# Performance work log

Measured on AMD Instinct MI355X. Metric: run time of the kernel, lower is better.

The kernel has to match this reference:

```python
import jax, jax.numpy as jnp
import numpy as np

B, C, N, OUT, K = 8, 64, 4096, 64, 16


def setup_inputs() -> dict:
    key = jax.random.key(0)
    k0, k1, k2, k3, k4 = jax.random.split(key, 5)
    x = jax.random.normal(k0, (B, C, N, 1), jnp.float32)
    s1 = 1.0 / np.sqrt(2 * C)
    s2 = 1.0 / np.sqrt(OUT)
    W1 = jax.random.uniform(k1, (2 * C, OUT), jnp.float32, -s1, s1)
    b1 = jax.random.uniform(k2, (OUT,), jnp.float32, -s1, s1)
    W2 = jax.random.uniform(k3, (OUT, OUT), jnp.float32, -s2, s2)
    b2 = jax.random.uniform(k4, (OUT,), jnp.float32, -s2, s2)
    return {"x": x, "W1": W1, "b1": b1, "W2": W2, "b2": b2}


def reference(x, W1, b1, W2, b2):
    # x: [B, C, N, 1] -> node features [B, N, C]
    xb = x[..., 0].transpose(0, 2, 1)  # [B, N, C]
    # kNN per batch element (PyG knn includes the point itself)
    sq = jnp.sum(xb * xb, axis=-1)  # [B, N]
    d2 = sq[:, :, None] + sq[:, None, :] - 2.0 * jnp.einsum('bnc,bmc->bnm', xb, xb)
    _, idx = jax.lax.top_k(-d2, K)  # [B, N, K] neighbor indices
    # gather neighbor features: [B, N, K, C]
    xj = jax.vmap(lambda f, i: jnp.take(f, i, axis=0))(xb, idx)
    xi = xb[:, :, None, :]  # [B, N, 1, C]
    # EdgeConv edge features: [x_i, x_j - x_i]
    e = jnp.concatenate([jnp.broadcast_to(xi, xj.shape), xj - xi], axis=-1)  # [B,N,K,2C]
    h = jax.nn.relu(e @ W1 + b1)
    h = jax.nn.relu(h @ W2 + b2)
    out = jnp.max(h, axis=2)  # max aggregation over neighbors -> [B, N, OUT]
    return out.transpose(0, 2, 1)[..., None]  # [B, OUT, N, 1]
```

## Files before the change

kernel.cpp:

```cpp
#include <hip/hip_runtime.h>
#include <stdint.h>

#define BB 8
#define CCH 64
#define NPB 4096
#define NPTS (BB*NPB)
#define PPW 8

typedef float  f32x2  __attribute__((ext_vector_type(2)));
typedef float  f32x4v __attribute__((ext_vector_type(4)));
typedef short  bf16x8 __attribute__((ext_vector_type(8)));
typedef unsigned short u16x8 __attribute__((ext_vector_type(8)));
typedef unsigned long long u64;
typedef unsigned int u32;

__device__ __forceinline__ unsigned short f2bf(float x) {
    u32 u = __float_as_uint(x);
    u += 0x7FFFu + ((u >> 16) & 1u);
    return (unsigned short)(u >> 16);
}

template<typename T>
__device__ __forceinline__ void sort16(T* key) {
#pragma unroll
    for (int kk = 2; kk <= 16; kk <<= 1) {
#pragma unroll
        for (int j = kk >> 1; j > 0; j >>= 1) {
#pragma unroll
            for (int i = 0; i < 16; ++i) {
                int l = i ^ j;
                if (l > i) {
                    bool up = ((i & kk) == 0);
                    T a = key[i], c = key[l];
                    bool cond = up ? (c < a) : (a < c);
                    key[i] = cond ? c : a;
                    key[l] = cond ? a : c;
                }
            }
        }
    }
}

template<typename T>
__device__ __forceinline__ void merge16(T* list, const T* key) {
    T m[16];
#pragma unroll
    for (int i = 0; i < 16; ++i) {
        T a = list[i], c = key[15 - i];
        m[i] = (c < a) ? c : a;
    }
#pragma unroll
    for (int j = 8; j > 0; j >>= 1) {
#pragma unroll
        for (int i = 0; i < 16; ++i) {
            if ((i & j) == 0) {
                T a = m[i], c = m[i + j];
                bool cond = c < a;
                m[i]     = cond ? c : a;
                m[i + j] = cond ? a : c;
            }
        }
    }
#pragma unroll
    for (int i = 0; i < 16; ++i) list[i] = m[i];
}

__global__ void k_transpose(const float* __restrict__ x, float* __restrict__ xb,
                            unsigned short* __restrict__ xh, float* __restrict__ sq) {
    __shared__ float tile[64][65];
    int b  = blockIdx.y;
    int n0 = blockIdx.x * 64;
    int tx = threadIdx.x, ty = threadIdx.y;
    const float* xp = x + (size_t)b * CCH * NPB;
#pragma unroll
    for (int r = 0; r < 8; ++r) {
        int c = ty + r * 8;
        tile[c][tx] = xp[(size_t)c * NPB + n0 + tx];
    }
    __syncthreads();
    float* xbp = xb + ((size_t)b * NPB + n0) * CCH;
    unsigned short* xhp = xh + ((size_t)b * NPB + n0) * CCH;
    float* sqp = sq + (size_t)b * NPB + n0;
#pragma unroll
    for (int r = 0; r < 8; ++r) {
        int nn = ty + r * 8;
        float v = tile[tx][nn];
        xbp[(size_t)nn * CCH + tx] = v;
        xhp[(size_t)nn * CCH + tx] = f2bf(v);
        float s = v * v;
#pragma unroll
        for (int o = 32; o > 0; o >>= 1) s += __shfl_xor(s, o);
        if (tx == 0) sqp[nn] = s;
    }
}

__global__ void k_prepw(const float* __restrict__ W1, const float* __restrict__ W2,
                        unsigned short* __restrict__ W1t, unsigned short* __restrict__ W2t) {
    int t = blockIdx.x * 256 + threadIdx.x;
    if (t < 8192) {
        int o = t >> 7, k = t & 127;
        float v = (k < 64) ? (W1[k * 64 + o] - W1[(64 + k) * 64 + o]) : W1[k * 64 + o];
        W1t[o * 128 + k] = f2bf(v);
    } else if (t < 12288) {
        int u = t - 8192;
        int o = u >> 6, j = u & 63;
        W2t[o * 64 + j] = f2bf(W2[j * 64 + o]);
    }
}

__global__ __launch_bounds__(256) void k_gemm(const unsigned short* __restrict__ xh,
                                              const float* __restrict__ sq,
                                              u32* __restrict__ cand) {
    __shared__ float dtile[64][65];
    __shared__ u32 llist[64][65];
    int b = blockIdx.y >> 6;
    const unsigned short* xhB = xh + (size_t)b * NPB * CCH;
    const float* sqB = sq + (size_t)b * NPB;
    u32* candB = cand + (size_t)b * 64 * NPB * 16;
    int l = threadIdx.x & 63;
    int w = threadIdx.x >> 6;
    int m0 = (blockIdx.y & 63) * 64;
    int n0 = blockIdx.x * 64;
    const unsigned short* ap = xhB + (size_t)(m0 + w * 16 + (l & 15)) * CCH + ((l >> 4) * 8);
    bf16x8 a0 = *(const bf16x8*)ap;
    bf16x8 a1 = *(const bf16x8*)(ap + 32);
    f32x4v z = {0.f, 0.f, 0.f, 0.f};
    f32x4v acc[4];
#pragma unroll
    for (int cg = 0; cg < 4; ++cg) {
        const unsigned short* bp = xhB + (size_t)(n0 + cg * 16 + (l & 15)) * CCH + ((l >> 4) * 8);
        bf16x8 b0 = *(const bf16x8*)bp;
        bf16x8 b1 = *(const bf16x8*)(bp + 32);
        acc[cg] = __builtin_amdgcn_mfma_f32_16x16x32_bf16(a0, b0, z, 0, 0, 0);
        acc[cg] = __builtin_amdgcn_mfma_f32_16x16x32_bf16(a1, b1, acc[cg], 0, 0, 0);
    }
    int rb = m0 + w * 16 + (l >> 4) * 4;
    float4 sr = *(const float4*)(sqB + rb);
    float sqr[4] = {sr.x, sr.y, sr.z, sr.w};
#pragma unroll
    for (int cg = 0; cg < 4; ++cg) {
        int cit = cg * 16 + (l & 15);
        float sc = sqB[n0 + cit];
#pragma unroll
        for (int j = 0; j < 4; ++j) {
            float v = fmaxf(fmaf(-2.f, acc[cg][j], sqr[j] + sc), 0.f);
            dtile[w * 16 + (l >> 4) * 4 + j][cit] = v;
        }
    }
    __syncthreads();
    {
        int row = l, ch = w;
        u32 key[16];
#pragma unroll
        for (int e = 0; e < 16; ++e) {
            float v = dtile[row][ch * 16 + e];
            key[e] = ((u32)f2bf(v) << 16) | (u32)(n0 + ch * 16 + e);
        }
        sort16(key);
#pragma unroll
        for (int i = 0; i < 16; ++i) llist[row][ch * 16 + i] = key[i];
    }
    __syncthreads();
    if (threadIdx.x < 64) {
        int r2 = threadIdx.x;
        u32 list[16], tmp[16];
#pragma unroll
        for (int i = 0; i < 16; ++i) list[i] = llist[r2][i];
#pragma unroll
        for (int ch2 = 1; ch2 < 4; ++ch2) {
#pragma unroll
            for (int i = 0; i < 16; ++i) tmp[i] = llist[r2][ch2 * 16 + i];
            merge16(list, tmp);
        }
        u32* cp = candB + ((size_t)blockIdx.x * NPB + (m0 + r2)) * 16;
#pragma unroll
        for (int i = 0; i < 16; ++i) cp[i] = list[i];
    }
}

__global__ __launch_bounds__(256, 1) void k_post(const u32* __restrict__ cand,
                                                 const float* __restrict__ xb,
                                                 const float* __restrict__ sq,
                                                 int* __restrict__ idxo) {
    __shared__ u32 slots[4][64];
    int l  = threadIdx.x & 63;
    int rl = __builtin_amdgcn_readfirstlane(threadIdx.x >> 6);
    int rowg = blockIdx.x * 4 + rl;
    int b    = rowg >> 12;
    int row  = rowg & 4095;
    const float* xbB = xb + ((size_t)b << 12) * CCH;
    const float* sqB = sq + ((size_t)b << 12);
    const u32* candB = cand + (size_t)b * 64 * NPB * 16;
    const float* xr = xbB + (size_t)row * CCH;
    float rr[64];
#pragma unroll
    for (int i = 0; i < 16; ++i) {
        float4 v = *(const float4*)(xr + i * 4);
        rr[4*i] = v.x; rr[4*i+1] = v.y; rr[4*i+2] = v.z; rr[4*i+3] = v.w;
    }
    u32 karr[16];
    {
        const uint4* cp = (const uint4*)(candB + ((size_t)l * NPB + row) * 16);
#pragma unroll
        for (int i = 0; i < 4; ++i) {
            uint4 v = cp[i];
            karr[4*i] = v.x; karr[4*i+1] = v.y; karr[4*i+2] = v.z; karr[4*i+3] = v.w;
        }
    }
    u32 lo = 0, hi = 0xFFFFu;
#pragma unroll
    for (int it = 0; it < 16; ++it) {
        u32 mid = (lo + hi) >> 1;
        int c = 0;
#pragma unroll
        for (int i = 0; i < 16; ++i) c += ((karr[i] >> 16) <= mid) ? 1 : 0;
#pragma unroll
        for (int o = 32; o > 0; o >>= 1) c += __shfl_xor(c, o);
        bool ge = (c >= 48);
        lo = ge ? lo : (mid + 1);
        hi = ge ? mid : hi;
    }
    u32 vstar = hi;
    int cnt = 0;
#pragma unroll
    for (int i = 0; i < 16; ++i) cnt += ((karr[i] >> 16) <= vstar) ? 1 : 0;
    int pre = cnt;
#pragma unroll
    for (int d = 1; d < 64; d <<= 1) {
        int t = __shfl_up(pre, d);
        if (l >= d) pre += t;
    }
    int base = pre - cnt;
    u32* sl = slots[rl];
    sl[l] = 0xFFFFFFFFu;
#pragma unroll
    for (int i = 0; i < 16; ++i) {
        if (i < cnt) {
            int s = base + i;
            if (s < 64) sl[s] = karr[i];
        }
    }
    u32 mk = sl[l];
    u64 key = ~0ULL;
    if (mk != 0xFFFFFFFFu) {
        int col = (int)(mk & 0xFFFFu);
        const float* xj = xbB + (size_t)col * CCH;
        float lod = 0.f, hid = 0.f;
#pragma unroll
        for (int q = 0; q < 8; ++q) {
            float4 v  = *(const float4*)(xj + q * 4);
            float4 wv = *(const float4*)(xj + 32 + q * 4);
            lod = fmaf(v.x,  rr[4*q+0], lod);
            lod = fmaf(v.y,  rr[4*q+1], lod);
            lod = fmaf(v.z,  rr[4*q+2], lod);
            lod = fmaf(v.w,  rr[4*q+3], lod);
            hid = fmaf(wv.x, rr[32+4*q+0], hid);
            hid = fmaf(wv.y, rr[32+4*q+1], hid);
            hid = fmaf(wv.z, rr[32+4*q+2], hid);
            hid = fmaf(wv.w, rr[32+4*q+3], hid);
        }
        float d = fmaf(-2.f, lod + hid, sqB[col]);
        u32 fb = __float_as_uint(d);
        fb ^= (fb >> 31) ? 0xFFFFFFFFu : 0x80000000u;
        key = ((u64)fb << 32) | (u32)col;
    }
#pragma unroll
    for (int kk = 2; kk <= 64; kk <<= 1) {
#pragma unroll
        for (int j = kk >> 1; j > 0; j >>= 1) {
            u64 p = (u64)__shfl_xor((long long)key, j);
            bool keep_min = (((l & kk) == 0) == ((l & j) == 0));
            bool plt = p < key;
            key = keep_min ? (plt ? p : key) : (plt ? key : p);
        }
    }
    if (l < 16) idxo[(size_t)rowg * 16 + l] = (int)(key & 0xFFFFFFFFu);
}

__global__ __launch_bounds__(256, 1) void k_mlp2(const unsigned short* __restrict__ xh,
                                                 const int* __restrict__ idx,
                                                 const unsigned short* __restrict__ W1t,
                                                 const unsigned short* __restrict__ W2t,
                                                 const float* __restrict__ b1,
                                                 const float* __restrict__ b2,
                                                 float* __restrict__ out) {
    __shared__ unsigned short h1l[4][16 * 72];
    int l   = threadIdx.x & 63;
    int wib = threadIdx.x >> 6;
    int e   = l & 15;
    int kg  = l >> 4;
    int wave = blockIdx.x * 4 + wib;
    unsigned short* hl = h1l[wib];

    bf16x8 w1f[4][4];
#pragma unroll
    for (int nt = 0; nt < 4; ++nt)
#pragma unroll
        for (int s = 0; s < 4; ++s)
            w1f[nt][s] = *(const bf16x8*)(W1t + (size_t)(nt * 16 + e) * 128 + s * 32 + kg * 8);
    bf16x8 w2f[4][2];
#pragma unroll
    for (int nt = 0; nt < 4; ++nt)
#pragma unroll
        for (int s = 0; s < 2; ++s)
            w2f[nt][s] = *(const bf16x8*)(W2t + (size_t)(nt * 16 + e) * 64 + s * 32 + kg * 8);
    float b1v[4], b2v[4];
#pragma unroll
    for (int nt = 0; nt < 4; ++nt) { b1v[nt] = b1[nt * 16 + e]; b2v[nt] = b2[nt * 16 + e]; }

    int p0 = wave * PPW;
    int bb = p0 >> 12;
    int n0 = p0 & 4095;
    const unsigned short* xhB = xh + ((size_t)bb << 12) * CCH;
    f32x4v z = {0.f, 0.f, 0.f, 0.f};
    float mx[4][PPW];
#pragma unroll
    for (int nt = 0; nt < 4; ++nt)
#pragma unroll
        for (int pi = 0; pi < PPW; ++pi) mx[nt][pi] = 0.f;

#pragma unroll
    for (int pi = 0; pi < PPW; ++pi) {
        int n = n0 + pi;
        int je = idx[((size_t)(p0 + pi)) * 16 + e];
        bf16x8 a[4];
        a[0] = *(const bf16x8*)(xhB + (size_t)n * 64 + kg * 8);
        a[1] = *(const bf16x8*)(xhB + (size_t)n * 64 + 32 + kg * 8);
        a[2] = *(const bf16x8*)(xhB + (size_t)je * 64 + kg * 8);
        a[3] = *(const bf16x8*)(xhB + (size_t)je * 64 + 32 + kg * 8);
#pragma unroll
        for (int nt = 0; nt < 4; ++nt) {
            f32x4v acc = z;
#pragma unroll
            for (int s = 0; s < 4; ++s)
                acc = __builtin_amdgcn_mfma_f32_16x16x32_bf16(a[s], w1f[nt][s], acc, 0, 0, 0);
#pragma unroll
            for (int j = 0; j < 4; ++j) {
                float h = fmaxf(acc[j] + b1v[nt], 0.f);
                hl[(kg * 4 + j) * 72 + nt * 16 + e] = f2bf(h);
            }
        }
        bf16x8 a2[2];
        a2[0] = *(const bf16x8*)(hl + (size_t)e * 72 + kg * 8);
        a2[1] = *(const bf16x8*)(hl + (size_t)e * 72 + 32 + kg * 8);
#pragma unroll
        for (int nt = 0; nt < 4; ++nt) {
            f32x4v acc = z;
            acc = __builtin_amdgcn_mfma_f32_16x16x32_bf16(a2[0], w2f[nt][0], acc, 0, 0, 0);
            acc = __builtin_amdgcn_mfma_f32_16x16x32_bf16(a2[1], w2f[nt][1], acc, 0, 0, 0);
            float m4 = 0.f;
#pragma unroll
            for (int j = 0; j < 4; ++j)
                m4 = fmaxf(m4, fmaxf(acc[j] + b2v[nt], 0.f));
            mx[nt][pi] = m4;
        }
    }
#pragma unroll
    for (int nt = 0; nt < 4; ++nt)
#pragma unroll
        for (int pi = 0; pi < PPW; ++pi) {
            float v = mx[nt][pi];
            v = fmaxf(v, __shfl_xor(v, 16));
            v = fmaxf(v, __shfl_xor(v, 32));
            mx[nt][pi] = v;
        }
    if (kg == 0) {
#pragma unroll
        for (int nt = 0; nt < 4; ++nt) {
            float* op = out + ((size_t)bb * 64 + nt * 16 + e) * NPB + n0;
#pragma unroll
            for (int pi = 0; pi < PPW; ++pi) op[pi] = mx[nt][pi];
        }
    }
}

extern "C" void kernel_launch(void* const* d_in, const int* in_sizes, int n_in,
                              void* d_out, int out_size, void* d_ws, size_t ws_size,
                              hipStream_t stream) {
    const float* x  = (const float*)d_in[0];
    const float* W1 = (const float*)d_in[1];
    const float* b1 = (const float*)d_in[2];
    const float* W2 = (const float*)d_in[3];
    const float* b2 = (const float*)d_in[4];
    float* out = (float*)d_out;

    const size_t MB = 1024 * 1024;
    char* ws = (char*)d_ws;
    float*          xb  = (float*)(ws);
    unsigned short* xh  = (unsigned short*)(ws + 8 * MB);
    float*          sq  = (float*)(ws + 12 * MB);
    unsigned short* W1t = (unsigned short*)(ws + 12 * MB + 256 * 1024);
    unsigned short* W2t = (unsigned short*)(ws + 12 * MB + 272 * 1024);
    u32*            cand = (u32*)(ws + 13 * MB);
    size_t candAll = (size_t)BB * 64 * NPB * 16 * 4;
    size_t needF = 13 * MB + candAll + (size_t)NPTS * 16 * 4;

    hipLaunchKernelGGL(k_transpose, dim3(NPB / 64, BB), dim3(64, 8), 0, stream, x, xb, xh, sq);
    hipLaunchKernelGGL(k_prepw, dim3(48), dim3(256), 0, stream, W1, W2, W1t, W2t);

    if (ws_size >= needF + MB) {
        int* idxb = (int*)(ws + 13 * MB + candAll);
        hipLaunchKernelGGL(k_gemm, dim3(NPB / 64, 64 * BB), dim3(256), 0, stream,
                           xh, sq, cand);
        hipLaunchKernelGGL(k_post, dim3(NPTS / 4), dim3(256), 0, stream,
                           cand, xb, sq, idxb);
        hipLaunchKernelGGL(k_mlp2, dim3(NPTS / PPW / 4), dim3(256), 0, stream,
                           xh, idxb, W1t, W2t, b1, b2, out);
    } else {
        int* idxb = (int*)(ws + 30 * MB);
        for (int b = 0; b < BB; ++b) {
            const unsigned short* xhB = xh + (size_t)b * NPB * CCH;
            const float* xbB = xb + (size_t)b * NPB * CCH;
            const float* sqB = sq + (size_t)b * NPB;
            hipLaunchKernelGGL(k_gemm, dim3(NPB / 64, 64), dim3(256), 0, stream,
                               xhB, sqB, cand);
            hipLaunchKernelGGL(k_post, dim3(NPB / 4), dim3(256), 0, stream,
                               cand, xbB, sqB, idxb + (size_t)b * NPB * 16);
        }
        hipLaunchKernelGGL(k_mlp2, dim3(NPTS / PPW / 4), dim3(256), 0, stream,
                           xh, idxb, W1t, W2t, b1, b2, out);
    }
}
```

Baseline: 322.6 us.

## Write full bf16 distance matrix and select top-k by radix threshold in post kernel

The GEMM kernel no longer sorts and merges per-tile top-16 candidate lists. It writes the whole bf16 distance matrix to workspace, and the post kernel finds the 48th-smallest threshold by binary search over all 4096 distances per row, with tie handling. This removes the bitonic sort and merge work and the wide candidate buffer. In exchange it writes and reads a 256MB distance matrix and does 64-element count loops per lane. The launch logic is restructured, and if the workspace is too small for even the per-batch path, no kNN stage runs at all.

```diff
diff --git a/kernel.cpp b/kernel.cpp
--- a/kernel.cpp
+++ b/kernel.cpp
@@ -18,51 +18,6 @@
     u32 u = __float_as_uint(x);
     u += 0x7FFFu + ((u >> 16) & 1u);
     return (unsigned short)(u >> 16);
-}
-
-template<typename T>
-__device__ __forceinline__ void sort16(T* key) {
-#pragma unroll
-    for (int kk = 2; kk <= 16; kk <<= 1) {
-#pragma unroll
-        for (int j = kk >> 1; j > 0; j >>= 1) {
-#pragma unroll
-            for (int i = 0; i < 16; ++i) {
-                int l = i ^ j;
-                if (l > i) {
-                    bool up = ((i & kk) == 0);
-                    T a = key[i], c = key[l];
-                    bool cond = up ? (c < a) : (a < c);
-                    key[i] = cond ? c : a;
-                    key[l] = cond ? a : c;
-                }
-            }
-        }
-    }
-}
-
-template<typename T>
-__device__ __forceinline__ void merge16(T* list, const T* key) {
-    T m[16];
-#pragma unroll
-    for (int i = 0; i < 16; ++i) {
-        T a = list[i], c = key[15 - i];
-        m[i] = (c < a) ? c : a;
-    }
-#pragma unroll
-    for (int j = 8; j > 0; j >>= 1) {
-#pragma unroll
-        for (int i = 0; i < 16; ++i) {
-            if ((i & j) == 0) {
-                T a = m[i], c = m[i + j];
-                bool cond = c < a;
-                m[i]     = cond ? c : a;
-                m[i + j] = cond ? a : c;
-            }
-        }
-    }
-#pragma unroll
-    for (int i = 0; i < 16; ++i) list[i] = m[i];
 }
 
 __global__ void k_transpose(const float* __restrict__ x, float* __restrict__ xb,
@@ -110,13 +65,11 @@
 
 __global__ __launch_bounds__(256) void k_gemm(const unsigned short* __restrict__ xh,
                                               const float* __restrict__ sq,
-                                              u32* __restrict__ cand) {
-    __shared__ float dtile[64][65];
-    __shared__ u32 llist[64][65];
+                                              unsigned short* __restrict__ dt) {
+    __shared__ float dtile[64][68];
     int b = blockIdx.y >> 6;
     const unsigned short* xhB = xh + (size_t)b * NPB * CCH;
     const float* sqB = sq + (size_t)b * NPB;
-    u32* candB = cand + (size_t)b * 64 * NPB * 16;
     int l = threadIdx.x & 63;
     int w = threadIdx.x >> 6;
     int m0 = (blockIdx.y & 63) * 64;
@@ -148,37 +101,21 @@
         }
     }
     __syncthreads();
-    {
-        int row = l, ch = w;
-        u32 key[16];
-#pragma unroll
-        for (int e = 0; e < 16; ++e) {
-            float v = dtile[row][ch * 16 + e];
-            key[e] = ((u32)f2bf(v) << 16) | (u32)(n0 + ch * 16 + e);
-        }
-        sort16(key);
-#pragma unroll
-        for (int i = 0; i < 16; ++i) llist[row][ch * 16 + i] = key[i];
-    }
-    __syncthreads();
-    if (threadIdx.x < 64) {
-        int r2 = threadIdx.x;
-        u32 list[16], tmp[16];
-#pragma unroll
-        for (int i = 0; i < 16; ++i) list[i] = llist[r2][i];
-#pragma unroll
-        for (int ch2 = 1; ch2 < 4; ++ch2) {
-#pragma unroll
-            for (int i = 0; i < 16; ++i) tmp[i] = llist[r2][ch2 * 16 + i];
-            merge16(list, tmp);
-        }
-        u32* cp = candB + ((size_t)blockIdx.x * NPB + (m0 + r2)) * 16;
-#pragma unroll
-        for (int i = 0; i < 16; ++i) cp[i] = list[i];
-    }
-}
-
-__global__ __launch_bounds__(256, 1) void k_post(const u32* __restrict__ cand,
+    int row = threadIdx.x >> 2;
+    int c0  = (threadIdx.x & 3) * 16;
+    const float4* dr = (const float4*)(&dtile[row][c0]);
+    float4 v0 = dr[0], v1 = dr[1], v2 = dr[2], v3 = dr[3];
+    u16x8 o0, o1;
+    o0[0] = f2bf(v0.x); o0[1] = f2bf(v0.y); o0[2] = f2bf(v0.z); o0[3] = f2bf(v0.w);
+    o0[4] = f2bf(v1.x); o0[5] = f2bf(v1.y); o0[6] = f2bf(v1.z); o0[7] = f2bf(v1.w);
+    o1[0] = f2bf(v2.x); o1[1] = f2bf(v2.y); o1[2] = f2bf(v2.z); o1[3] = f2bf(v2.w);
+    o1[4] = f2bf(v3.x); o1[5] = f2bf(v3.y); o1[6] = f2bf(v3.z); o1[7] = f2bf(v3.w);
+    size_t base = ((size_t)(b * NPB + m0 + row)) * NPB + n0 + c0;
+    *(u16x8*)(dt + base)     = o0;
+    *(u16x8*)(dt + base + 8) = o1;
+}
+
+__global__ __launch_bounds__(256, 1) void k_post(const unsigned short* __restrict__ dt,
                                                  const float* __restrict__ xb,
                                                  const float* __restrict__ sq,
                                                  int* __restrict__ idxo) {
@@ -190,7 +127,6 @@
     int row  = rowg & 4095;
     const float* xbB = xb + ((size_t)b << 12) * CCH;
     const float* sqB = sq + ((size_t)b << 12);
-    const u32* candB = cand + (size_t)b * 64 * NPB * 16;
     const float* xr = xbB + (size_t)row * CCH;
     float rr[64];
 #pragma unroll
@@ -198,22 +134,23 @@
         float4 v = *(const float4*)(xr + i * 4);
         rr[4*i] = v.x; rr[4*i+1] = v.y; rr[4*i+2] = v.z; rr[4*i+3] = v.w;
     }
-    u32 karr[16];
+    u32 va[64];
     {
-        const uint4* cp = (const uint4*)(candB + ((size_t)l * NPB + row) * 16);
-#pragma unroll
-        for (int i = 0; i < 4; ++i) {
-            uint4 v = cp[i];
-            karr[4*i] = v.x; karr[4*i+1] = v.y; karr[4*i+2] = v.z; karr[4*i+3] = v.w;
-        }
-    }
-    u32 lo = 0, hi = 0xFFFFu;
-#pragma unroll
-    for (int it = 0; it < 16; ++it) {
+        const u16x8* dp = (const u16x8*)(dt + (size_t)rowg * NPB + l * 64);
+#pragma unroll
+        for (int i = 0; i < 8; ++i) {
+            u16x8 v = dp[i];
+#pragma unroll
+            for (int e = 0; e < 8; ++e) va[i * 8 + e] = (u32)v[e];
+        }
+    }
+    u32 lo = 0, hi = 0x7FFFu;
+#pragma unroll
+    for (int it = 0; it < 15; ++it) {
         u32 mid = (lo + hi) >> 1;
         int c = 0;
 #pragma unroll
-        for (int i = 0; i < 16; ++i) c += ((karr[i] >> 16) <= mid) ? 1 : 0;
+        for (int i = 0; i < 64; ++i) c += (va[i] <= mid) ? 1 : 0;
 #pragma unroll
         for (int o = 32; o > 0; o >>= 1) c += __shfl_xor(c, o);
         bool ge = (c >= 48);
@@ -221,23 +158,35 @@
         hi = ge ? mid : hi;
     }
     u32 vstar = hi;
-    int cnt = 0;
-#pragma unroll
-    for (int i = 0; i < 16; ++i) cnt += ((karr[i] >> 16) <= vstar) ? 1 : 0;
-    int pre = cnt;
+    int cs = 0, ct = 0;
+#pragma unroll
+    for (int i = 0; i < 64; ++i) {
+        cs += (va[i] < vstar) ? 1 : 0;
+        ct += (va[i] == vstar) ? 1 : 0;
+    }
+    int ps = cs, pt = ct;
 #pragma unroll
     for (int d = 1; d < 64; d <<= 1) {
-        int t = __shfl_up(pre, d);
-        if (l >= d) pre += t;
-    }
-    int base = pre - cnt;
+        int ts = __shfl_up(ps, d);
+        int tt = __shfl_up(pt, d);
+        if (l >= d) { ps += ts; pt += tt; }
+    }
+    int baseS = ps - cs;
+    int baseT = pt - ct;
+    int totS = __shfl(ps, 63);
     u32* sl = slots[rl];
     sl[l] = 0xFFFFFFFFu;
-#pragma unroll
-    for (int i = 0; i < 16; ++i) {
-        if (i < cnt) {
-            int s = base + i;
-            if (s < 64) sl[s] = karr[i];
+    int ks = 0, kt = 0;
+#pragma unroll
+    for (int i = 0; i < 64; ++i) {
+        u32 v = va[i];
+        if (v < vstar) {
+            sl[baseS + ks] = (v << 16) | (u32)(l * 64 + i);
+            ks++;
+        } else if (v == vstar) {
+            int s = totS + baseT + kt;
+            if (s < 64) sl[s] = (v << 16) | (u32)(l * 64 + i);
+            kt++;
         }
     }
     u32 mk = sl[l];
@@ -391,33 +340,27 @@
     float*          sq  = (float*)(ws + 12 * MB);
     unsigned short* W1t = (unsigned short*)(ws + 12 * MB + 256 * 1024);
     unsigned short* W2t = (unsigned short*)(ws + 12 * MB + 272 * 1024);
-    u32*            cand = (u32*)(ws + 13 * MB);
-    size_t candAll = (size_t)BB * 64 * NPB * 16 * 4;
-    size_t needF = 13 * MB + candAll + (size_t)NPTS * 16 * 4;
+    int*            idxb = (int*)(ws + 13 * MB);
+    unsigned short* dt  = (unsigned short*)(ws + 16 * MB);
+    size_t needFull = 16 * MB + (size_t)NPTS * NPB * 2 + MB;
+    size_t needBat  = 16 * MB + (size_t)NPB * NPB * 2 + MB;
 
     hipLaunchKernelGGL(k_transpose, dim3(NPB / 64, BB), dim3(64, 8), 0, stream, x, xb, xh, sq);
     hipLaunchKernelGGL(k_prepw, dim3(48), dim3(256), 0, stream, W1, W2, W1t, W2t);
 
-    if (ws_size >= needF + MB) {
-        int* idxb = (int*)(ws + 13 * MB + candAll);
-        hipLaunchKernelGGL(k_gemm, dim3(NPB / 64, 64 * BB), dim3(256), 0, stream,
-                           xh, sq, cand);
-        hipLaunchKernelGGL(k_post, dim3(NPTS / 4), dim3(256), 0, stream,
-                           cand, xb, sq, idxb);
-        hipLaunchKernelGGL(k_mlp2, dim3(NPTS / PPW / 4), dim3(256), 0, stream,
-                           xh, idxb, W1t, W2t, b1, b2, out);
-    } else {
-        int* idxb = (int*)(ws + 30 * MB);
+    if (ws_size >= needFull) {
+        hipLaunchKernelGGL(k_gemm, dim3(NPB / 64, 64 * BB), dim3(256), 0, stream, xh, sq, dt);
+        hipLaunchKernelGGL(k_post, dim3(NPTS / 4), dim3(256), 0, stream, dt, xb, sq, idxb);
+    } else if (ws_size >= needBat) {
         for (int b = 0; b < BB; ++b) {
             const unsigned short* xhB = xh + (size_t)b * NPB * CCH;
             const float* xbB = xb + (size_t)b * NPB * CCH;
             const float* sqB = sq + (size_t)b * NPB;
-            hipLaunchKernelGGL(k_gemm, dim3(NPB / 64, 64), dim3(256), 0, stream,
-                               xhB, sqB, cand);
+            hipLaunchKernelGGL(k_gemm, dim3(NPB / 64, 64), dim3(256), 0, stream, xhB, sqB, dt);
             hipLaunchKernelGGL(k_post, dim3(NPB / 4), dim3(256), 0, stream,
-                               cand, xbB, sqB, idxb + (size_t)b * NPB * 16);
-        }
-        hipLaunchKernelGGL(k_mlp2, dim3(NPTS / PPW / 4), dim3(256), 0, stream,
-                           xh, idxb, W1t, W2t, b1, b2, out);
-    }
-}
+                               dt, xbB, sqB, idxb + (size_t)b * NPB * 16);
+        }
+    }
+    hipLaunchKernelGGL(k_mlp2, dim3(NPTS / PPW / 4), dim3(256), 0, stream,
+                       xh, idxb, W1t, W2t, b1, b2, out);
+}
```

After: 571.2 us. +77.1%, slower.
